# Kernel optimization log

Measured on AMD Instinct MI355X. Metric: run time of the kernel, lower is better.

The kernel has to match this reference:

```python
import jax, jax.numpy as jnp
import numpy as np

B, CIN, COUT, H, W = 4, 256, 256, 64, 64
DG, K, PAD = 4, 3, 1  # deformable groups, kernel size, padding
KK = K * K


def setup_inputs() -> dict:
    key = jax.random.key(0)
    k1, k2, k3, k4 = jax.random.split(key, 4)
    x = jax.random.normal(k1, (B, CIN, H, W), jnp.float32)
    shape = jax.random.normal(k2, (B, 2, H, W), jnp.float32)
    # conv_offset: Conv2d(2, DG*2*K*K, 3, pad=1, bias=False), init std=0.1
    w_offset = jax.random.normal(k3, (DG * 2 * KK, 2, K, K), jnp.float32) * 0.1
    # deform conv weight: [COUT, CIN, K, K], init std=0.01
    w_deform = jax.random.normal(k4, (COUT, CIN, K, K), jnp.float32) * 0.01
    return {"x": x, "shape": shape, "w_offset": w_offset, "w_deform": w_deform}


def _conv2d(x, w, pad):
    return jax.lax.conv_general_dilated(
        x, w, window_strides=(1, 1), padding=[(pad, pad), (pad, pad)],
        dimension_numbers=("NCHW", "OIHW", "NCHW"))


def _deform_conv(x, offset, w):
    """DCN v1 (mmcv DeformConv, stride=1, dilation=1, groups=1)."""
    Bn, C, Hh, Ww = x.shape
    Cg = C // DG
    # offset channel layout: [DG, KK, (dy, dx)]
    off = offset.reshape(Bn, DG, KK, 2, Hh, Ww)
    dy, dx = off[:, :, :, 0], off[:, :, :, 1]          # [B, DG, KK, H, W]
    ky, kx = jnp.meshgrid(jnp.arange(K), jnp.arange(K), indexing="ij")
    # base sampling grid: p0 + pn  (stride 1, pad PAD)
    grid_y = ky.reshape(KK, 1, 1) + jnp.arange(Hh).reshape(1, Hh, 1) - PAD  # [KK,H,1]
    grid_x = kx.reshape(KK, 1, 1) + jnp.arange(Ww).reshape(1, 1, Ww) - PAD  # [KK,1,W]
    sy = dy + grid_y[None, None].astype(dy.dtype)       # [B, DG, KK, H, W]
    sx = dx + grid_x[None, None].astype(dx.dtype)

    y0 = jnp.floor(sy)
    x0 = jnp.floor(sx)
    ly = (sy - y0).reshape(Bn, DG, 1, -1)               # [B, DG, 1, KK*H*W]
    lx = (sx - x0).reshape(Bn, DG, 1, -1)
    y0i = y0.astype(jnp.int32)
    x0i = x0.astype(jnp.int32)

    xg = x.reshape(Bn, DG, Cg, Hh * Ww)                 # per-group channels

    def corner(yi, xi):
        valid = (yi >= 0) & (yi <= Hh - 1) & (xi >= 0) & (xi <= Ww - 1)
        yc = jnp.clip(yi, 0, Hh - 1)
        xc = jnp.clip(xi, 0, Ww - 1)
        idx = (yc * Ww + xc).reshape(Bn, DG, -1)        # [B, DG, KK*H*W]
        v = jnp.take_along_axis(xg, idx[:, :, None, :], axis=3)  # [B,DG,Cg,KK*H*W]
        return v * valid.reshape(Bn, DG, 1, -1).astype(v.dtype)

    v00 = corner(y0i, x0i)
    v01 = corner(y0i, x0i + 1)
    v10 = corner(y0i + 1, x0i)
    v11 = corner(y0i + 1, x0i + 1)
    val = (v00 * (1 - ly) * (1 - lx) + v01 * (1 - ly) * lx
           + v10 * ly * (1 - lx) + v11 * ly * lx)       # [B, DG, Cg, KK*H*W]

    # im2col columns -> GEMM with weight
    cols = val.reshape(Bn, C * KK, Hh * Ww)
    out = jnp.einsum("oc,bcp->bop", w.reshape(w.shape[0], C * KK), cols)
    return out.reshape(Bn, w.shape[0], Hh, Ww)


def reference(x, shape, w_offset, w_deform):
    offset = _conv2d(shape, w_offset, PAD)              # [B, DG*2*KK, H, W]
    return jax.nn.relu(_deform_conv(x, offset, w_deform))
```

## Files before the change

kernel.cpp:

```cpp
#include <hip/hip_runtime.h>
#include <hip/hip_bf16.h>
#include <stdint.h>

typedef __attribute__((ext_vector_type(8))) short bf16x8;
typedef __attribute__((ext_vector_type(4))) float f32x4;
typedef __attribute__((ext_vector_type(4))) unsigned int u32x4;

__device__ __forceinline__ float u2f(unsigned int u) {
  union { unsigned int i; float f; } c; c.i = u; return c.f;
}
__device__ __forceinline__ unsigned int f2b(float f) {
  union { float f; unsigned int i; } c; c.f = f;
  unsigned int x = c.i;
  return (x + 0x7fffu + ((x >> 16) & 1u)) >> 16;
}

__global__ __launch_bounds__(256) void k_prep(
    const float* __restrict__ shape, const float* __restrict__ w_off,
    const float* __restrict__ x, const float* __restrict__ wd,
    char* __restrict__ desc, unsigned short* __restrict__ xt,
    unsigned short* __restrict__ wp) {
  __shared__ float tile[64][65];
  int bid = blockIdx.x;
  int t = threadIdx.x;
  if (bid < 576) {
    int band = bid & 3;
    int rem = bid >> 2;
    int b = rem / 36, r2 = rem % 36, g = r2 / 9, kk = r2 % 9;
    int ky = kk / 3, kx = kk - ky * 3;
    int ocy = g * 18 + kk * 2;
    float wy[18], wx[18];
#pragma unroll
    for (int i = 0; i < 18; ++i) { wy[i] = w_off[ocy * 18 + i]; wx[i] = w_off[(ocy + 1) * 18 + i]; }
    const float* sp = shape + (size_t)b * 2 * 4096;
    char* dp = desc + (size_t)rem * 4096 * 32;
#pragma unroll
    for (int e = 0; e < 4; ++e) {
      int p = band * 1024 + t * 4 + e;
      int y = p >> 6, xx0 = p & 63;
      float dy = 0.f, dx = 0.f;
#pragma unroll
      for (int ic = 0; ic < 2; ++ic)
#pragma unroll
        for (int kyy = 0; kyy < 3; ++kyy) {
          int yy = y + kyy - 1;
          if (yy < 0 || yy > 63) continue;
#pragma unroll
          for (int kxx = 0; kxx < 3; ++kxx) {
            int xx = xx0 + kxx - 1;
            if (xx < 0 || xx > 63) continue;
            float sv = sp[ic * 4096 + yy * 64 + xx];
            dy += sv * wy[ic * 9 + kyy * 3 + kxx];
            dx += sv * wx[ic * 9 + kyy * 3 + kxx];
          }
        }
      float sy = dy + (float)(y + ky - 1);
      float sx = dx + (float)(xx0 + kx - 1);
      float fy = floorf(sy), fx = floorf(sx);
      float ly = sy - fy, lx = sx - fx;
      int y0 = (int)fy, x0 = (int)fx;
      float vy0 = (y0 >= 0 && y0 <= 63) ? 1.f : 0.f;
      float vy1 = (y0 >= -1 && y0 <= 62) ? 1.f : 0.f;
      float vx0 = (x0 >= 0 && x0 <= 63) ? 1.f : 0.f;
      float vx1 = (x0 >= -1 && x0 <= 62) ? 1.f : 0.f;
      float w00 = (1.f - ly) * (1.f - lx) * vy0 * vx0;
      float w01 = (1.f - ly) * lx * vy0 * vx1;
      float w10 = ly * (1.f - lx) * vy1 * vx0;
      float w11 = ly * lx * vy1 * vx1;
      unsigned int yc0 = (unsigned int)min(max(y0, 0), 63);
      unsigned int yc1 = (unsigned int)min(max(y0 + 1, 0), 63);
      unsigned int xc0 = (unsigned int)min(max(x0, 0), 63);
      unsigned int xc1 = (unsigned int)min(max(x0 + 1, 0), 63);
      unsigned int gb = (unsigned int)(g * 128);
      u32x4 offs;
      offs[0] = (yc0 * 64 + xc0) * 512 + gb;
      offs[1] = (yc0 * 64 + xc1) * 512 + gb;
      offs[2] = (yc1 * 64 + xc0) * 512 + gb;
      offs[3] = (yc1 * 64 + xc1) * 512 + gb;
      uint2 wpk;
      wpk.x = f2b(w00) | (f2b(w01) << 16);
      wpk.y = f2b(w10) | (f2b(w11) << 16);
      char* r = dp + (size_t)p * 32;
      *(u32x4*)(r) = offs;
      *(uint2*)(r + 16) = wpk;
    }
  } else if (bid < 1600) {
    int id = bid - 576;
    int b = id >> 8, ct = (id >> 6) & 3, pt = id & 63;
    int c0 = ct * 64, p0 = pt * 64;
#pragma unroll
    for (int i = 0; i < 4; ++i) {
      int row = (t >> 4) + i * 16;
      int seg = t & 15;
      float4 v = *(const float4*)&x[(size_t)(b * 256 + c0 + row) * 4096 + p0 + seg * 4];
      tile[row][seg * 4 + 0] = v.x;
      tile[row][seg * 4 + 1] = v.y;
      tile[row][seg * 4 + 2] = v.z;
      tile[row][seg * 4 + 3] = v.w;
    }
    __syncthreads();
    {
      int pl = t >> 2;
      int cs = (t & 3) * 16;
      unsigned int wbuf[8];
#pragma unroll
      for (int j = 0; j < 8; ++j)
        wbuf[j] = f2b(tile[cs + 2 * j][pl]) | (f2b(tile[cs + 2 * j + 1][pl]) << 16);
      unsigned short* dst = xt + (size_t)(b * 4096 + p0 + pl) * 256 + c0 + cs;
      *(u32x4*)(dst) = *(u32x4*)&wbuf[0];
      *(u32x4*)(dst + 8) = *(u32x4*)&wbuf[4];
    }
  } else {
    int id = (bid - 1600) * 256 + t;
    int m = id >> 8, ci = id & 255;
    int g = ci >> 6, c = ci & 63;
    int cs = c ^ ((m & 7) << 3);
    const float* src = wd + (size_t)(m * 256 + ci) * 9;
    float v[9];
#pragma unroll
    for (int kk = 0; kk < 9; ++kk) v[kk] = src[kk];
#pragma unroll
    for (int kk = 0; kk < 9; ++kk)
      wp[(size_t)(kk * 4 + g) * 16384 + m * 64 + cs] = (unsigned short)f2b(v[kk]);
  }
}

struct CSet { uint2 v0, v1, v2, v3; uint2 w; };

#define DESC_LD(c, dvo, dvw) do { \
    const char* rp_ = descb + (size_t)((((c) & 3) * 9 + ((c) >> 2))) * (4096 * 32); \
    dvo = *(const u32x4*)(rp_); \
    dvw = *(const uint2*)(rp_ + 16); \
  } while (0)

#define CORNERS(S, dvo, dvw) do { \
    (S).v0 = *(const uint2*)(xtbB + (dvo)[0] + cb16); \
    (S).v1 = *(const uint2*)(xtbB + (dvo)[1] + cb16); \
    (S).v2 = *(const uint2*)(xtbB + (dvo)[2] + cb16); \
    (S).v3 = *(const uint2*)(xtbB + (dvo)[3] + cb16); \
    (S).w = (dvw); \
  } while (0)

#define BLEND(S, bbuf) do { \
    float w0_ = u2f((S).w.x << 16), w1_ = u2f((S).w.x & 0xffff0000u); \
    float w2_ = u2f((S).w.y << 16), w3_ = u2f((S).w.y & 0xffff0000u); \
    float lo0 = 0.f, hi0 = 0.f, lo1 = 0.f, hi1 = 0.f; \
    lo0 += w0_ * u2f((S).v0.x << 16); hi0 += w0_ * u2f((S).v0.x & 0xffff0000u); \
    lo1 += w0_ * u2f((S).v0.y << 16); hi1 += w0_ * u2f((S).v0.y & 0xffff0000u); \
    lo0 += w1_ * u2f((S).v1.x << 16); hi0 += w1_ * u2f((S).v1.x & 0xffff0000u); \
    lo1 += w1_ * u2f((S).v1.y << 16); hi1 += w1_ * u2f((S).v1.y & 0xffff0000u); \
    lo0 += w2_ * u2f((S).v2.x << 16); hi0 += w2_ * u2f((S).v2.x & 0xffff0000u); \
    lo1 += w2_ * u2f((S).v2.y << 16); hi1 += w2_ * u2f((S).v2.y & 0xffff0000u); \
    lo0 += w3_ * u2f((S).v3.x << 16); hi0 += w3_ * u2f((S).v3.x & 0xffff0000u); \
    lo1 += w3_ * u2f((S).v3.y << 16); hi1 += w3_ * u2f((S).v3.y & 0xffff0000u); \
    uint2 o_; \
    o_.x = f2b(lo0) | (f2b(hi0) << 16); \
    o_.y = f2b(lo1) | (f2b(hi1) << 16); \
    *(uint2*)((bbuf) + bwr) = o_; \
  } while (0)

#define STAGE_A(c, abuf) do { \
    const unsigned short* asrc_ = wp + (size_t)(c) * 16384 + t * 8; \
    _Pragma("unroll") for (int i_ = 0; i_ < 4; ++i_) \
      __builtin_amdgcn_global_load_lds( \
          (const __attribute__((address_space(1))) unsigned int*)(asrc_ + i_ * 4096), \
          (__attribute__((address_space(3))) unsigned int*)((abuf) + t * 16 + i_ * 8192), \
          16, 0, 0); \
  } while (0)

#define MFMA_STEP(abuf, bbuf) do { \
    _Pragma("unroll") for (int ks_ = 0; ks_ < 2; ++ks_) { \
      int kb_ = ks_ * 64 + kq; \
      bf16x8 a0_ = *(const bf16x8*)((abuf) + (wid * 32 + lm) * 128 + (kb_ ^ swz)); \
      bf16x8 a1_ = *(const bf16x8*)((abuf) + (wid * 32 + 16 + lm) * 128 + (kb_ ^ swz)); \
      bf16x8 b0_ = *(const bf16x8*)((bbuf) + lm * 128 + (kb_ ^ swz)); \
      bf16x8 b1_ = *(const bf16x8*)((bbuf) + (16 + lm) * 128 + (kb_ ^ swz)); \
      acc00 = __builtin_amdgcn_mfma_f32_16x16x32_bf16(a0_, b0_, acc00, 0, 0, 0); \
      acc01 = __builtin_amdgcn_mfma_f32_16x16x32_bf16(a0_, b1_, acc01, 0, 0, 0); \
      acc10 = __builtin_amdgcn_mfma_f32_16x16x32_bf16(a1_, b0_, acc10, 0, 0, 0); \
      acc11 = __builtin_amdgcn_mfma_f32_16x16x32_bf16(a1_, b1_, acc11, 0, 0, 0); \
    } \
  } while (0)

#define PHASE(c, Acur, Anext, Bnext, Sfill, Sblend, dvoF, dvwF, dvoU, dvwU) do { \
    int cs_ = (c) + 1 < 36 ? (c) + 1 : 35; \
    int cd_ = (c) + 3 < 36 ? (c) + 3 : 35; \
    STAGE_A(cs_, Anext); \
    CORNERS(Sfill, dvoU, dvwU); \
    DESC_LD(cd_, dvoF, dvwF); \
    MFMA_STEP(Acur, (Bnext) == ldsB0 ? ldsB1 : ldsB0); \
    BLEND(Sblend, Bnext); \
    asm volatile("s_waitcnt lgkmcnt(0)" ::: "memory"); \
    asm volatile("s_waitcnt vmcnt(6)" ::: "memory"); \
    __builtin_amdgcn_s_barrier(); \
  } while (0)

__global__ __launch_bounds__(512, 4) void k_deform_main(
    const unsigned short* __restrict__ xt, const unsigned short* __restrict__ wp,
    const char* __restrict__ desc, float* __restrict__ out) {
  __shared__ __align__(16) char lds[73728];
  const int t = threadIdx.x;
  const int l = t & 63;
  const int wid = t >> 6;

  int orig = blockIdx.x;
  int bid = (orig & 7) * 64 + (orig >> 3);
  const int xh = bid & 1;
  const int rowid = bid >> 1;
  const int b = rowid >> 6;
  const int y = rowid & 63;

  const int p = t >> 4;
  const int cq = t & 15;
  const int xg = xh * 32 + p;
  const int cb16 = cq * 8;
  const int bwr = p * 128 + ((cq * 8) ^ ((p & 7) << 4));

  const int lm = l & 15;
  const int kq = (l >> 4) << 4;
  const int swz = (lm & 7) << 4;

  f32x4 acc00 = {}, acc01 = {}, acc10 = {}, acc11 = {};

  const char* descb = desc + (size_t)(b * 36 * 4096 + y * 64 + xg) * 32;
  const char* xtbB = (const char*)(xt + (size_t)b * 4096 * 256);

  char* ldsA0 = lds;
  char* ldsA1 = lds + 32768;
  char* ldsB0 = lds + 65536;
  char* ldsB1 = lds + 69632;

  CSet SE, SO;
  u32x4 dvoE, dvoO;
  uint2 dvwE, dvwO;

  {
    u32x4 o0, o1; uint2 w0p, w1p;
    DESC_LD(0, o0, w0p);
    DESC_LD(1, o1, w1p);
    DESC_LD(2, dvoO, dvwO);
    STAGE_A(0, ldsA0);
    CSet S0;
    CORNERS(S0, o0, w0p);
    CORNERS(SO, o1, w1p);
    BLEND(S0, ldsB0);
    asm volatile("s_waitcnt lgkmcnt(0)" ::: "memory");
    asm volatile("s_waitcnt vmcnt(4)" ::: "memory");
    __builtin_amdgcn_s_barrier();
  }

  for (int pr = 0; pr < 18; ++pr) {
    const int c0 = pr * 2;
    PHASE(c0,     ldsA0, ldsA1, ldsB1, SE, SO, dvoE, dvwE, dvoO, dvwO);
    PHASE(c0 + 1, ldsA1, ldsA0, ldsB0, SO, SE, dvoO, dvwO, dvoE, dvwE);
  }

  const int lm4 = (l >> 4) << 2;
  float* ob = out + (size_t)(b * 256 + wid * 32) * 4096 + y * 64 + xh * 32;
#pragma unroll
  for (int r = 0; r < 4; ++r) {
    ob[(size_t)(lm4 + r) * 4096 + lm] = fmaxf(acc00[r], 0.f);
    ob[(size_t)(lm4 + r) * 4096 + 16 + lm] = fmaxf(acc01[r], 0.f);
    ob[(size_t)(16 + lm4 + r) * 4096 + lm] = fmaxf(acc10[r], 0.f);
    ob[(size_t)(16 + lm4 + r) * 4096 + 16 + lm] = fmaxf(acc11[r], 0.f);
  }
}

extern "C" void kernel_launch(void* const* d_in, const int* in_sizes, int n_in,
                              void* d_out, int out_size, void* d_ws, size_t ws_size,
                              hipStream_t stream) {
  const float* x     = (const float*)d_in[0];
  const float* shape = (const float*)d_in[1];
  const float* w_off = (const float*)d_in[2];
  const float* w_def = (const float*)d_in[3];
  float* out = (float*)d_out;
  char* ws = (char*)d_ws;

  char* desc          = ws;
  unsigned short* xt  = (unsigned short*)(ws + 18874368);
  unsigned short* wpk = (unsigned short*)(ws + 18874368 + 8388608);

  k_prep<<<1856, 256, 0, stream>>>(shape, w_off, x, w_def, desc, xt, wpk);
  k_deform_main<<<512, 512, 0, stream>>>(xt, wpk, desc, out);
}
```

Before: 78.58 us.

## Load weight fragments directly into registers and widen block to full output row

The weight operand is no longer staged through LDS with async global-to-LDS copies. Each wave now loads its A fragments straight from global memory into registers, double-buffered across phases, and the weight packing drops its swizzle to match. Each block grows to 1024 threads covering a full 64-pixel row, with waves split 8x2 over output channels and pixels. This shrinks LDS use and halves the grid, meant to cut LDS traffic and barrier cost, but it adds register pressure and uncoalesced global weight reads, and 256 blocks may underfill the GPU.

```diff
diff --git a/kernel.cpp b/kernel.cpp
--- a/kernel.cpp
+++ b/kernel.cpp
@@ -114,14 +114,13 @@
     int id = (bid - 1600) * 256 + t;
     int m = id >> 8, ci = id & 255;
     int g = ci >> 6, c = ci & 63;
-    int cs = c ^ ((m & 7) << 3);
     const float* src = wd + (size_t)(m * 256 + ci) * 9;
     float v[9];
 #pragma unroll
     for (int kk = 0; kk < 9; ++kk) v[kk] = src[kk];
 #pragma unroll
     for (int kk = 0; kk < 9; ++kk)
-      wp[(size_t)(kk * 4 + g) * 16384 + m * 64 + cs] = (unsigned short)f2b(v[kk]);
+      wp[(size_t)(kk * 4 + g) * 16384 + m * 64 + c] = (unsigned short)f2b(v[kk]);
   }
 }
 
@@ -159,77 +158,77 @@
     *(uint2*)((bbuf) + bwr) = o_; \
   } while (0)
 
-#define STAGE_A(c, abuf) do { \
-    const unsigned short* asrc_ = wp + (size_t)(c) * 16384 + t * 8; \
-    _Pragma("unroll") for (int i_ = 0; i_ < 4; ++i_) \
-      __builtin_amdgcn_global_load_lds( \
-          (const __attribute__((address_space(1))) unsigned int*)(asrc_ + i_ * 4096), \
-          (__attribute__((address_space(3))) unsigned int*)((abuf) + t * 16 + i_ * 8192), \
-          16, 0, 0); \
-  } while (0)
-
-#define MFMA_STEP(abuf, bbuf) do { \
-    _Pragma("unroll") for (int ks_ = 0; ks_ < 2; ++ks_) { \
-      int kb_ = ks_ * 64 + kq; \
-      bf16x8 a0_ = *(const bf16x8*)((abuf) + (wid * 32 + lm) * 128 + (kb_ ^ swz)); \
-      bf16x8 a1_ = *(const bf16x8*)((abuf) + (wid * 32 + 16 + lm) * 128 + (kb_ ^ swz)); \
-      bf16x8 b0_ = *(const bf16x8*)((bbuf) + lm * 128 + (kb_ ^ swz)); \
-      bf16x8 b1_ = *(const bf16x8*)((bbuf) + (16 + lm) * 128 + (kb_ ^ swz)); \
-      acc00 = __builtin_amdgcn_mfma_f32_16x16x32_bf16(a0_, b0_, acc00, 0, 0, 0); \
-      acc01 = __builtin_amdgcn_mfma_f32_16x16x32_bf16(a0_, b1_, acc01, 0, 0, 0); \
-      acc10 = __builtin_amdgcn_mfma_f32_16x16x32_bf16(a1_, b0_, acc10, 0, 0, 0); \
-      acc11 = __builtin_amdgcn_mfma_f32_16x16x32_bf16(a1_, b1_, acc11, 0, 0, 0); \
-    } \
-  } while (0)
-
-#define PHASE(c, Acur, Anext, Bnext, Sfill, Sblend, dvoF, dvwF, dvoU, dvwU) do { \
-    int cs_ = (c) + 1 < 36 ? (c) + 1 : 35; \
+#define LOAD_A(c, F) do { \
+    const unsigned short* ap_ = wpl + (size_t)(c) * 16384; \
+    F##0 = *(const bf16x8*)(ap_); \
+    F##1 = *(const bf16x8*)(ap_ + 1024); \
+    F##2 = *(const bf16x8*)(ap_ + 32); \
+    F##3 = *(const bf16x8*)(ap_ + 1056); \
+  } while (0)
+
+#define MFMA4(F, bbuf) do { \
+    bf16x8 b00_ = *(const bf16x8*)((bbuf) + brow0 + (kq ^ swz)); \
+    bf16x8 b10_ = *(const bf16x8*)((bbuf) + brow1 + (kq ^ swz)); \
+    acc00 = __builtin_amdgcn_mfma_f32_16x16x32_bf16(F##0, b00_, acc00, 0, 0, 0); \
+    acc01 = __builtin_amdgcn_mfma_f32_16x16x32_bf16(F##0, b10_, acc01, 0, 0, 0); \
+    acc10 = __builtin_amdgcn_mfma_f32_16x16x32_bf16(F##1, b00_, acc10, 0, 0, 0); \
+    acc11 = __builtin_amdgcn_mfma_f32_16x16x32_bf16(F##1, b10_, acc11, 0, 0, 0); \
+    bf16x8 b01_ = *(const bf16x8*)((bbuf) + brow0 + ((64 + kq) ^ swz)); \
+    bf16x8 b11_ = *(const bf16x8*)((bbuf) + brow1 + ((64 + kq) ^ swz)); \
+    acc00 = __builtin_amdgcn_mfma_f32_16x16x32_bf16(F##2, b01_, acc00, 0, 0, 0); \
+    acc01 = __builtin_amdgcn_mfma_f32_16x16x32_bf16(F##2, b11_, acc01, 0, 0, 0); \
+    acc10 = __builtin_amdgcn_mfma_f32_16x16x32_bf16(F##3, b01_, acc10, 0, 0, 0); \
+    acc11 = __builtin_amdgcn_mfma_f32_16x16x32_bf16(F##3, b11_, acc11, 0, 0, 0); \
+  } while (0)
+
+#define PHASE(c, AF, AG, Bcur, Bnext, Sfill, Sblend, dvoF, dvwF, dvoU, dvwU) do { \
+    int ca_ = (c) + 1 < 36 ? (c) + 1 : 35; \
     int cd_ = (c) + 3 < 36 ? (c) + 3 : 35; \
-    STAGE_A(cs_, Anext); \
+    LOAD_A(ca_, AG); \
     CORNERS(Sfill, dvoU, dvwU); \
     DESC_LD(cd_, dvoF, dvwF); \
-    MFMA_STEP(Acur, (Bnext) == ldsB0 ? ldsB1 : ldsB0); \
+    MFMA4(AF, Bcur); \
     BLEND(Sblend, Bnext); \
     asm volatile("s_waitcnt lgkmcnt(0)" ::: "memory"); \
-    asm volatile("s_waitcnt vmcnt(6)" ::: "memory"); \
     __builtin_amdgcn_s_barrier(); \
   } while (0)
 
-__global__ __launch_bounds__(512, 4) void k_deform_main(
+__global__ __launch_bounds__(1024, 4) void k_deform_main(
     const unsigned short* __restrict__ xt, const unsigned short* __restrict__ wp,
     const char* __restrict__ desc, float* __restrict__ out) {
-  __shared__ __align__(16) char lds[73728];
+  __shared__ __align__(16) char lds[16384];
   const int t = threadIdx.x;
   const int l = t & 63;
   const int wid = t >> 6;
+  const int wm = wid >> 1;
+  const int wn = wid & 1;
 
   int orig = blockIdx.x;
-  int bid = (orig & 7) * 64 + (orig >> 3);
-  const int xh = bid & 1;
-  const int rowid = bid >> 1;
-  const int b = rowid >> 6;
-  const int y = rowid & 63;
+  int bid = (orig & 7) * 32 + (orig >> 3);
+  const int b = bid >> 6;
+  const int y = bid & 63;
 
   const int p = t >> 4;
   const int cq = t & 15;
-  const int xg = xh * 32 + p;
   const int cb16 = cq * 8;
   const int bwr = p * 128 + ((cq * 8) ^ ((p & 7) << 4));
 
   const int lm = l & 15;
   const int kq = (l >> 4) << 4;
   const int swz = (lm & 7) << 4;
+  const int brow0 = (wn * 32 + lm) * 128;
+  const int brow1 = brow0 + 2048;
 
   f32x4 acc00 = {}, acc01 = {}, acc10 = {}, acc11 = {};
 
-  const char* descb = desc + (size_t)(b * 36 * 4096 + y * 64 + xg) * 32;
+  const char* descb = desc + (size_t)(b * 36 * 4096 + y * 64 + p) * 32;
   const char* xtbB = (const char*)(xt + (size_t)b * 4096 * 256);
-
-  char* ldsA0 = lds;
-  char* ldsA1 = lds + 32768;
-  char* ldsB0 = lds + 65536;
-  char* ldsB1 = lds + 69632;
-
+  const unsigned short* wpl = wp + (wm * 32 + lm) * 64 + ((l >> 4) << 3);
+
+  char* ldsB0 = lds;
+  char* ldsB1 = lds + 8192;
+
+  bf16x8 AFe0, AFe1, AFe2, AFe3, AFo0, AFo1, AFo2, AFo3;
   CSet SE, SO;
   u32x4 dvoE, dvoO;
   uint2 dvwE, dvwO;
@@ -239,24 +238,23 @@
     DESC_LD(0, o0, w0p);
     DESC_LD(1, o1, w1p);
     DESC_LD(2, dvoO, dvwO);
-    STAGE_A(0, ldsA0);
+    LOAD_A(0, AFe);
     CSet S0;
     CORNERS(S0, o0, w0p);
     CORNERS(SO, o1, w1p);
     BLEND(S0, ldsB0);
     asm volatile("s_waitcnt lgkmcnt(0)" ::: "memory");
-    asm volatile("s_waitcnt vmcnt(4)" ::: "memory");
     __builtin_amdgcn_s_barrier();
   }
 
   for (int pr = 0; pr < 18; ++pr) {
     const int c0 = pr * 2;
-    PHASE(c0,     ldsA0, ldsA1, ldsB1, SE, SO, dvoE, dvwE, dvoO, dvwO);
-    PHASE(c0 + 1, ldsA1, ldsA0, ldsB0, SO, SE, dvoO, dvwO, dvoE, dvwE);
+    PHASE(c0,     AFe, AFo, ldsB0, ldsB1, SE, SO, dvoE, dvwE, dvoO, dvwO);
+    PHASE(c0 + 1, AFo, AFe, ldsB1, ldsB0, SO, SE, dvoO, dvwO, dvoE, dvwE);
   }
 
   const int lm4 = (l >> 4) << 2;
-  float* ob = out + (size_t)(b * 256 + wid * 32) * 4096 + y * 64 + xh * 32;
+  float* ob = out + (size_t)(b * 256 + wm * 32) * 4096 + y * 64 + wn * 32;
 #pragma unroll
   for (int r = 0; r < 4; ++r) {
     ob[(size_t)(lm4 + r) * 4096 + lm] = fmaxf(acc00[r], 0.f);
@@ -281,5 +279,5 @@
   unsigned short* wpk = (unsigned short*)(ws + 18874368 + 8388608);
 
   k_prep<<<1856, 256, 0, stream>>>(shape, w_off, x, w_def, desc, xt, wpk);
-  k_deform_main<<<512, 512, 0, stream>>>(xt, wpk, desc, out);
-}
+  k_deform_main<<<256, 1024, 0, stream>>>(xt, wpk, desc, out);
+}
```

Result: slower. 119.5 us (+52.0%).
